# Kernel optimization log

Measured on AMD Instinct MI355X. Metric: run time of the kernel, lower is better.

Reference implementation:

```python
import jax, jax.numpy as jnp
import numpy as np


def squash(x, axis=-1):
    sq = jnp.sum(x * x, axis=axis, keepdims=True)
    return (sq / (1.0 + sq)) * (x / (jnp.sqrt(sq) + 1e-8))


def conv2d(x, w, b, stride):
    y = jax.lax.conv_general_dilated(x, w, (stride, stride), 'VALID',
                                     dimension_numbers=('NCHW', 'OIHW', 'NCHW'))
    return y + b[None, :, None, None]


def setup_inputs():
    key = jax.random.key(0)
    ks = jax.random.split(key, 8)
    B = 512
    return {
        'x': jax.random.uniform(ks[0], (B, 1, 28, 28), jnp.float32),
        'conv_w': 0.1 * jax.random.normal(ks[1], (256, 1, 9, 9), jnp.float32),
        'conv_b': jnp.zeros((256,), jnp.float32),
        'pc_w': 0.02 * jax.random.normal(ks[2], (256, 256, 9, 9), jnp.float32),
        'pc_b': jnp.zeros((256,), jnp.float32),
        'W_route': 0.01 * jax.random.normal(ks[3], (10, 1152, 16, 8), jnp.float32),
        'dec_w1': 0.05 * jax.random.normal(ks[4], (512, 160), jnp.float32),
        'dec_b1': jnp.zeros((512,), jnp.float32),
        'dec_w2': 0.05 * jax.random.normal(ks[5], (1024, 512), jnp.float32),
        'dec_b2': jnp.zeros((1024,), jnp.float32),
        'dec_w3': 0.05 * jax.random.normal(ks[6], (784, 1024), jnp.float32),
        'dec_b3': jnp.zeros((784,), jnp.float32),
    }


def capsnet_forward(x, conv_w, conv_b, pc_w, pc_b, W_route,
                    dec_w1, dec_b1, dec_w2, dec_b2, dec_w3, dec_b3,
                    num_routing=3):
    B = x.shape[0]
    # conv1 + relu: [B,1,28,28] -> [B,256,20,20]
    h = jax.nn.relu(conv2d(x, conv_w, conv_b, 1))
    # primary caps conv: [B,256,20,20] -> [B,256,6,6]
    p = conv2d(h, pc_w, pc_b, 2)
    # reshape (C,H,W flattened, grouped by capsule dim 8) -> [B,1152,8], squash
    caps = squash(p.reshape(B, -1, 8))
    # u_hat[b,o,n,d] = sum_i W[o,n,d,i] * caps[b,n,i]  -> [B,10,1152,16]
    u_hat = jnp.einsum('ondi,bni->bond', W_route, caps)
    u_hat_d = jax.lax.stop_gradient(u_hat)
    # dynamic routing
    b_logit = jnp.zeros((B, 10, 1152), u_hat.dtype)
    for _ in range(num_routing - 1):
        c = jax.nn.softmax(b_logit, axis=1)              # over out caps
        s = jnp.einsum('bond,bon->bod', u_hat_d, c)      # [B,10,16]
        v = squash(s)
        b_logit = b_logit + jnp.einsum('bond,bod->bon', u_hat_d, v)
    c = jax.nn.softmax(b_logit, axis=1)
    s = jnp.einsum('bond,bon->bod', u_hat, c)
    v = squash(s)                                        # [B,10,16]
    logits = jnp.linalg.norm(v, axis=-1)                 # [B,10]
    pred = jax.nn.one_hot(jnp.argmax(logits, axis=-1), 10, dtype=v.dtype)
    dec_in = (v * pred[..., None]).reshape(B, -1)        # [B,160]
    h1 = jax.nn.relu(dec_in @ dec_w1.T + dec_b1)
    h2 = jax.nn.relu(h1 @ dec_w2.T + dec_b2)
    reconstruction = jax.nn.sigmoid(h2 @ dec_w3.T + dec_b3)
    return logits, reconstruction


def reference(x, conv_w, conv_b, pc_w, pc_b, W_route,
              dec_w1, dec_b1, dec_w2, dec_b2, dec_w3, dec_b3):
    return capsnet_forward(x, conv_w, conv_b, pc_w, pc_b, W_route,
                           dec_w1, dec_b1, dec_w2, dec_b2, dec_w3, dec_b3)
```

## Files before the change

kernel.cpp:

```cpp
#include <hip/hip_runtime.h>
#include <math.h>


typedef _Float16 f16x8 __attribute__((ext_vector_type(8)));
typedef float f32x4 __attribute__((ext_vector_type(4)));

__global__ __launch_bounds__(256) void k_conv1(const float* __restrict__ x,
        const float* __restrict__ w, const float* __restrict__ bias,
        _Float16* __restrict__ ahi, _Float16* __restrict__ alo) {
    __shared__ __align__(16) float xs[784];
    const int b = blockIdx.x;
    const int t = threadIdx.x;
    for (int i = t; i < 784; i += 256) xs[i] = x[b * 784 + i];
    __syncthreads();

    float wr[81];
#pragma unroll
    for (int i = 0; i < 81; ++i) wr[i] = w[t * 81 + i];
    const float bv = bias[t];

    for (int oy = 0; oy < 20; ++oy) {
        float acc[20];
#pragma unroll
        for (int px = 0; px < 20; ++px) acc[px] = bv;
#pragma unroll
        for (int ky = 0; ky < 9; ++ky) {
            const float* xrow = &xs[(oy + ky) * 28];
            float xr[28];
#pragma unroll
            for (int j = 0; j < 7; ++j) {
                float4 v4 = *(const float4*)(xrow + j * 4);
                xr[j * 4 + 0] = v4.x; xr[j * 4 + 1] = v4.y;
                xr[j * 4 + 2] = v4.z; xr[j * 4 + 3] = v4.w;
            }
#pragma unroll
            for (int kx = 0; kx < 9; ++kx) {
                const float wv = wr[ky * 9 + kx];
#pragma unroll
                for (int px = 0; px < 20; ++px)
                    acc[px] = fmaf(wv, xr[px + kx], acc[px]);
            }
        }
#pragma unroll
        for (int px = 0; px < 20; ++px) {
            const float v16 = fmaxf(acc[px], 0.f) * 16.f;
            const _Float16 hi = (_Float16)v16;
            const _Float16 lo = (_Float16)(v16 - (float)hi);
            const int idx = (b * 400 + oy * 20 + px) * 256 + t;
            ahi[idx] = hi;
            alo[idx] = lo;
        }
    }
}

__global__ __launch_bounds__(256) void k_wcvt(const float* __restrict__ w2,
        _Float16* __restrict__ whi, _Float16* __restrict__ wlo) {
    const int i = blockIdx.x * 256 + threadIdx.x;
    const int n = i / 20736;
    const int r = i - n * 20736;
    const int tap = r >> 8;
    const int ci = r & 255;
    const float v = w2[(n * 256 + ci) * 81 + tap] * 16.f;
    const _Float16 hi = (_Float16)v;
    whi[i] = hi;
    wlo[i] = (_Float16)(v - (float)hi);
}

__global__ __launch_bounds__(256) void k_pinit(const float* __restrict__ bias,
        float* __restrict__ p) {
    const int idx = blockIdx.x * 256 + threadIdx.x;
    const int q = idx / 36;
    p[idx] = bias[q & 255];
}

__global__ __launch_bounds__(256, 2) void k_conv2m(
        const _Float16* __restrict__ ahi, const _Float16* __restrict__ alo,
        const _Float16* __restrict__ whi, const _Float16* __restrict__ wlo,
        float* __restrict__ p) {
    __shared__ __align__(16) _Float16 lds[32768];
    _Float16* sAhi = lds;
    _Float16* sAlo = lds + 8192;
    _Float16* sBhi = lds + 16384;
    _Float16* sBlo = lds + 24576;

    const int t = threadIdx.x;
    const int l = t & 63, w = t >> 6;
    const int m0 = blockIdx.x * 128;
    const int n0 = blockIdx.y * 128;
    const int kz = blockIdx.z;

    const int oct = ((t & 7) ^ ((t >> 3) & 7)) * 8;
    int apix[4], wbase[4];
#pragma unroll
    for (int i = 0; i < 4; ++i) {
        const int r = i * 32 + (t >> 3);
        const int m = m0 + r;
        const int b = m / 36, pix = m - b * 36;
        const int oy = pix / 6, ox = pix - oy * 6;
        apix[i] = (b * 400 + oy * 40 + ox * 2) * 256 + oct;
        wbase[i] = (n0 + r) * 20736 + oct;
    }

    f32x4 acc[4][4];
#pragma unroll
    for (int mf = 0; mf < 4; ++mf)
#pragma unroll
        for (int nf = 0; nf < 4; ++nf) acc[mf][nf] = (f32x4){0.f, 0.f, 0.f, 0.f};

    const int wm = (w >> 1) * 64, wn = (w & 1) * 64;
    const int lm = l & 15, lk = l >> 4;

    f16x8 rAh[4], rAl[4], rBh[4], rBl[4];

#define C2_LOAD(s) do { \
        const int tap_ = (s) >> 2; \
        const int ci0_ = ((s) & 3) << 6; \
        const int ky_ = tap_ / 9, kx_ = tap_ - ky_ * 9; \
        const int koff_ = (ky_ * 20 + kx_) * 256 + ci0_; \
        const int k0_ = (s) * 64; \
        _Pragma("unroll") \
        for (int i_ = 0; i_ < 4; ++i_) { \
            rAh[i_] = *(const f16x8*)(ahi + apix[i_] + koff_); \
            rAl[i_] = *(const f16x8*)(alo + apix[i_] + koff_); \
            rBh[i_] = *(const f16x8*)(whi + wbase[i_] + k0_); \
            rBl[i_] = *(const f16x8*)(wlo + wbase[i_] + k0_); \
        } \
    } while (0)

    C2_LOAD(kz);

    for (int j = 0; j < 162; ++j) {
        __syncthreads();
#pragma unroll
        for (int i = 0; i < 4; ++i) {
            *(f16x8*)(sAhi + i * 2048 + t * 8) = rAh[i];
            *(f16x8*)(sAlo + i * 2048 + t * 8) = rAl[i];
            *(f16x8*)(sBhi + i * 2048 + t * 8) = rBh[i];
            *(f16x8*)(sBlo + i * 2048 + t * 8) = rBl[i];
        }
        __syncthreads();
        if (j < 161) C2_LOAD(2 * (j + 1) + kz);

#pragma unroll
        for (int ks = 0; ks < 2; ++ks) {
            f16x8 afh[4], afl[4];
#pragma unroll
            for (int mf = 0; mf < 4; ++mf) {
                const int row = wm + mf * 16 + lm;
                const int off = row * 64 + ((ks * 4 + lk) ^ (lm & 7)) * 8;
                afh[mf] = *(const f16x8*)&sAhi[off];
                afl[mf] = *(const f16x8*)&sAlo[off];
            }
#pragma unroll
            for (int nf = 0; nf < 4; ++nf) {
                const int row = wn + nf * 16 + lm;
                const int off = row * 64 + ((ks * 4 + lk) ^ (lm & 7)) * 8;
                const f16x8 bh = *(const f16x8*)&sBhi[off];
                const f16x8 bl = *(const f16x8*)&sBlo[off];
#pragma unroll
                for (int mf = 0; mf < 4; ++mf) {
                    acc[mf][nf] = __builtin_amdgcn_mfma_f32_16x16x32_f16(
                        afh[mf], bh, acc[mf][nf], 0, 0, 0);
                    acc[mf][nf] = __builtin_amdgcn_mfma_f32_16x16x32_f16(
                        afh[mf], bl, acc[mf][nf], 0, 0, 0);
                    acc[mf][nf] = __builtin_amdgcn_mfma_f32_16x16x32_f16(
                        afl[mf], bh, acc[mf][nf], 0, 0, 0);
                }
            }
        }
    }
#undef C2_LOAD

#pragma unroll
    for (int nf = 0; nf < 4; ++nf) {
        const int n = n0 + wn + nf * 16 + lm;
#pragma unroll
        for (int mf = 0; mf < 4; ++mf) {
#pragma unroll
            for (int r = 0; r < 4; ++r) {
                const int m = m0 + wm + mf * 16 + lk * 4 + r;
                const int b = m / 36, pix = m - b * 36;
                atomicAdd(&p[(b * 256 + n) * 36 + pix],
                          acc[mf][nf][r] * (1.f / 256.f));
            }
        }
    }
}

__global__ __launch_bounds__(256) void k_squash(float* __restrict__ pc) {
    const long long i = (long long)blockIdx.x * 256 + threadIdx.x;
    float* p = pc + i * 8;
    float4 v0 = *(float4*)p;
    float4 v1 = *(float4*)(p + 4);
    const float sq = v0.x * v0.x + v0.y * v0.y + v0.z * v0.z + v0.w * v0.w
                   + v1.x * v1.x + v1.y * v1.y + v1.z * v1.z + v1.w * v1.w;
    const float sc = (sq / (1.f + sq)) / (sqrtf(sq) + 1e-8f);
    v0.x *= sc; v0.y *= sc; v0.z *= sc; v0.w *= sc;
    v1.x *= sc; v1.y *= sc; v1.z *= sc; v1.w *= sc;
    *(float4*)p = v0;
    *(float4*)(p + 4) = v1;
}

__global__ __launch_bounds__(128) void k_route(const float* __restrict__ caps,
        const float* __restrict__ W, const float* __restrict__ vsum,
        float* __restrict__ sp, int uniform) {
    const int b = blockIdx.x, nc = blockIdx.y;
    const int t = threadIdx.x;
    const int d = t & 15, g = t >> 4;
    __shared__ float vs[160];
    __shared__ float red[2][160];
    if (uniform == 0)
        for (int i = t; i < 160; i += 128) vs[i] = vsum[b * 160 + i];
    __syncthreads();

    float sacc[10];
#pragma unroll
    for (int o = 0; o < 10; ++o) sacc[o] = 0.f;

    for (int i = 0; i < 16; ++i) {
        const int n = nc * 128 + i * 8 + g;
        const float* cp = caps + ((long long)b * 1152 + n) * 8;
        const float4 ca = *(const float4*)cp;
        const float4 cb = *(const float4*)(cp + 4);
        float uv[10];
#pragma unroll
        for (int o = 0; o < 10; ++o) {
            const float* wp = W + (((long long)o * 1152 + n) * 16 + d) * 8;
            const float4 wa = *(const float4*)wp;
            const float4 wb = *(const float4*)(wp + 4);
            float s = wa.x * ca.x;
            s = fmaf(wa.y, ca.y, s); s = fmaf(wa.z, ca.z, s); s = fmaf(wa.w, ca.w, s);
            s = fmaf(wb.x, cb.x, s); s = fmaf(wb.y, cb.y, s); s = fmaf(wb.z, cb.z, s);
            s = fmaf(wb.w, cb.w, s);
            uv[o] = s;
        }
        float c[10];
        if (uniform) {
#pragma unroll
            for (int o = 0; o < 10; ++o) c[o] = 0.1f;
        } else {
            float dot[10];
#pragma unroll
            for (int o = 0; o < 10; ++o) {
                float xx = uv[o] * vs[o * 16 + d];
                xx += __shfl_xor(xx, 1);
                xx += __shfl_xor(xx, 2);
                xx += __shfl_xor(xx, 4);
                xx += __shfl_xor(xx, 8);
                dot[o] = xx;
            }
            float mx = dot[0];
#pragma unroll
            for (int o = 1; o < 10; ++o) mx = fmaxf(mx, dot[o]);
            float sum = 0.f;
#pragma unroll
            for (int o = 0; o < 10; ++o) { c[o] = expf(dot[o] - mx); sum += c[o]; }
            const float inv = 1.f / sum;
#pragma unroll
            for (int o = 0; o < 10; ++o) c[o] *= inv;
        }
#pragma unroll
        for (int o = 0; o < 10; ++o) sacc[o] = fmaf(c[o], uv[o], sacc[o]);
    }
#pragma unroll
    for (int o = 0; o < 10; ++o) {
        sacc[o] += __shfl_xor(sacc[o], 16);
        sacc[o] += __shfl_xor(sacc[o], 32);
    }
    const int wv = t >> 6;
    if ((t & 63) < 16) {
#pragma unroll
        for (int o = 0; o < 10; ++o) red[wv][o * 16 + d] = sacc[o];
    }
    __syncthreads();
    for (int i = t; i < 160; i += 128)
        sp[((long long)(b * 9 + nc)) * 160 + i] = red[0][i] + red[1][i];
}

__global__ __launch_bounds__(160) void k_squashv(const float* __restrict__ sp,
        float* __restrict__ vsum, float* __restrict__ vbuf, int first) {
    const int b = blockIdx.x, t = threadIdx.x;
    float s = 0.f;
#pragma unroll
    for (int ch = 0; ch < 9; ++ch) s += sp[((long long)(b * 9 + ch)) * 160 + t];
    float sq = s * s;
    sq += __shfl_xor(sq, 1);
    sq += __shfl_xor(sq, 2);
    sq += __shfl_xor(sq, 4);
    sq += __shfl_xor(sq, 8);
    const float sc = (sq / (1.f + sq)) / (sqrtf(sq) + 1e-8f);
    const float v = s * sc;
    vbuf[b * 160 + t] = v;
    vsum[b * 160 + t] = first ? v : (vsum[b * 160 + t] + v);
}

__global__ __launch_bounds__(64) void k_logits(const float* __restrict__ v,
        float* __restrict__ logits, float* __restrict__ dec_in) {
    const int b = blockIdx.x * 64 + threadIdx.x;
    const float* vp = v + (long long)b * 160;
    float nrm[10];
    int amax = 0;
    float best = -1.f;
#pragma unroll
    for (int o = 0; o < 10; ++o) {
        float s = 0.f;
#pragma unroll
        for (int dd = 0; dd < 16; ++dd) { const float xv = vp[o * 16 + dd]; s = fmaf(xv, xv, s); }
        nrm[o] = sqrtf(s);
        if (nrm[o] > best) { best = nrm[o]; amax = o; }
    }
#pragma unroll
    for (int o = 0; o < 10; ++o) logits[b * 10 + o] = nrm[o];
#pragma unroll
    for (int o = 0; o < 10; ++o)
#pragma unroll
        for (int dd = 0; dd < 16; ++dd)
            dec_in[(long long)b * 160 + o * 16 + dd] = (o == amax) ? vp[o * 16 + dd] : 0.f;
}

template <int ACT>
__global__ __launch_bounds__(256) void k_gemm(const float* __restrict__ A,
        const float* __restrict__ W, const float* __restrict__ bias,
        float* __restrict__ C, int N, int K) {
    __shared__ float As[16][68];
    __shared__ float Bs[16][68];
    const int m0 = blockIdx.x * 64, n0 = blockIdx.y * 64;
    const int t = threadIdx.x;
    const int kl = t & 15, rr = t >> 4;
    const int tm = t & 15, tn = t >> 4;

    float acc[4][4];
#pragma unroll
    for (int i = 0; i < 4; ++i)
#pragma unroll
        for (int j = 0; j < 4; ++j) acc[i][j] = 0.f;

    for (int k0 = 0; k0 < K; k0 += 16) {
#pragma unroll
        for (int i = 0; i < 4; ++i) {
            As[kl][rr + i * 16] = A[(m0 + rr + i * 16) * K + k0 + kl];
            const int n = n0 + rr + i * 16;
            Bs[kl][rr + i * 16] = (n < N) ? W[(long long)n * K + k0 + kl] : 0.f;
        }
        __syncthreads();
#pragma unroll
        for (int kk = 0; kk < 16; ++kk) {
            float a[4], bb[4];
#pragma unroll
            for (int i = 0; i < 4; ++i) a[i] = As[kk][tm * 4 + i];
#pragma unroll
            for (int j = 0; j < 4; ++j) bb[j] = Bs[kk][tn * 4 + j];
#pragma unroll
            for (int i = 0; i < 4; ++i)
#pragma unroll
                for (int j = 0; j < 4; ++j)
                    acc[i][j] = fmaf(a[i], bb[j], acc[i][j]);
        }
        __syncthreads();
    }
#pragma unroll
    for (int j = 0; j < 4; ++j) {
        const int n = n0 + tn * 4 + j;
        if (n < N) {
            const float bv = bias[n];
#pragma unroll
            for (int i = 0; i < 4; ++i) {
                const int m = m0 + tm * 4 + i;
                float xv = acc[i][j] + bv;
                if (ACT == 0) xv = fmaxf(xv, 0.f);
                else          xv = 1.f / (1.f + expf(-xv));
                C[(long long)m * N + n] = xv;
            }
        }
    }
}

extern "C" void kernel_launch(void* const* d_in, const int* in_sizes, int n_in,
                              void* d_out, int out_size, void* d_ws, size_t ws_size,
                              hipStream_t stream) {
    const float* x      = (const float*)d_in[0];
    const float* conv_w = (const float*)d_in[1];
    const float* conv_b = (const float*)d_in[2];
    const float* pc_w   = (const float*)d_in[3];
    const float* pc_b   = (const float*)d_in[4];
    const float* Wrt    = (const float*)d_in[5];
    const float* dw1    = (const float*)d_in[6];
    const float* db1    = (const float*)d_in[7];
    const float* dw2    = (const float*)d_in[8];
    const float* db2    = (const float*)d_in[9];
    const float* dw3    = (const float*)d_in[10];
    const float* db3    = (const float*)d_in[11];

    float* out = (float*)d_out;
    char* wsb  = (char*)d_ws;

    _Float16* ahi = (_Float16*)(wsb);
    _Float16* alo = (_Float16*)(wsb + 104857600);
    _Float16* whi = (_Float16*)(wsb + 209715200);
    _Float16* wlo = (_Float16*)(wsb + 220332032);
    float* caps = (float*)(wsb + 230948864);
    float* spart= (float*)(wsb);
    float* vsum = (float*)(wsb + 2949120);
    float* vbuf = (float*)(wsb + 3276800);
    float* din  = (float*)(wsb + 3604480);
    float* h1   = (float*)(wsb + 3932160);
    float* h2   = (float*)(wsb + 4980736);

    k_conv1<<<512, 256, 0, stream>>>(x, conv_w, conv_b, ahi, alo);
    k_wcvt<<<20736, 256, 0, stream>>>(pc_w, whi, wlo);
    k_pinit<<<18432, 256, 0, stream>>>(pc_b, caps);
    k_conv2m<<<dim3(144, 2, 2), 256, 0, stream>>>(ahi, alo, whi, wlo, caps);
    k_squash<<<2304, 256, 0, stream>>>(caps);

    k_route<<<dim3(512, 9), 128, 0, stream>>>(caps, Wrt, vsum, spart, 1);
    k_squashv<<<512, 160, 0, stream>>>(spart, vsum, vbuf, 1);
    k_route<<<dim3(512, 9), 128, 0, stream>>>(caps, Wrt, vsum, spart, 0);
    k_squashv<<<512, 160, 0, stream>>>(spart, vsum, vbuf, 0);
    k_route<<<dim3(512, 9), 128, 0, stream>>>(caps, Wrt, vsum, spart, 0);
    k_squashv<<<512, 160, 0, stream>>>(spart, vsum, vbuf, 0);

    k_logits<<<8, 64, 0, stream>>>(vbuf, out, din);

    k_gemm<0><<<dim3(8, 8),  256, 0, stream>>>(din, dw1, db1, h1, 512, 160);
    k_gemm<0><<<dim3(8, 16), 256, 0, stream>>>(h1,  dw2, db2, h2, 1024, 512);
    k_gemm<1><<<dim3(8, 13), 256, 0, stream>>>(h2,  dw3, db3, out + 5120, 784, 1024);
}
```

Baseline: 1.715 ms.

## Split conv1 rows across blocks, halve conv2 K-tile, restructure routing to reuse W in LDS

```diff
diff --git a/kernel.cpp b/kernel.cpp
--- a/kernel.cpp
+++ b/kernel.cpp
@@ -10,6 +10,7 @@
         _Float16* __restrict__ ahi, _Float16* __restrict__ alo) {
     __shared__ __align__(16) float xs[784];
     const int b = blockIdx.x;
+    const int oy0 = blockIdx.y * 4;
     const int t = threadIdx.x;
     for (int i = t; i < 784; i += 256) xs[i] = x[b * 784 + i];
     __syncthreads();
@@ -19,7 +20,7 @@
     for (int i = 0; i < 81; ++i) wr[i] = w[t * 81 + i];
     const float bv = bias[t];
 
-    for (int oy = 0; oy < 20; ++oy) {
+    for (int oy = oy0; oy < oy0 + 4; ++oy) {
         float acc[20];
 #pragma unroll
         for (int px = 0; px < 20; ++px) acc[px] = bv;
@@ -73,32 +74,34 @@
     p[idx] = bias[q & 255];
 }
 
-__global__ __launch_bounds__(256, 2) void k_conv2m(
+__global__ __launch_bounds__(256, 3) void k_conv2m(
         const _Float16* __restrict__ ahi, const _Float16* __restrict__ alo,
         const _Float16* __restrict__ whi, const _Float16* __restrict__ wlo,
         float* __restrict__ p) {
-    __shared__ __align__(16) _Float16 lds[32768];
+    __shared__ __align__(16) _Float16 lds[16384];
     _Float16* sAhi = lds;
-    _Float16* sAlo = lds + 8192;
-    _Float16* sBhi = lds + 16384;
-    _Float16* sBlo = lds + 24576;
+    _Float16* sAlo = lds + 4096;
+    _Float16* sBhi = lds + 8192;
+    _Float16* sBlo = lds + 12288;
 
     const int t = threadIdx.x;
     const int l = t & 63, w = t >> 6;
+    const int lm = l & 15, lk = l >> 4;
     const int m0 = blockIdx.x * 128;
     const int n0 = blockIdx.y * 128;
     const int kz = blockIdx.z;
 
-    const int oct = ((t & 7) ^ ((t >> 3) & 7)) * 8;
-    int apix[4], wbase[4];
-#pragma unroll
-    for (int i = 0; i < 4; ++i) {
-        const int r = i * 32 + (t >> 3);
-        const int m = m0 + r;
+    int abase[2], bbase[2];
+#pragma unroll
+    for (int i = 0; i < 2; ++i) {
+        const int slot = i * 256 + t;
+        const int row = slot >> 2, phys = slot & 3;
+        const int logk = phys ^ ((row >> 1) & 3);
+        const int m = m0 + row;
         const int b = m / 36, pix = m - b * 36;
         const int oy = pix / 6, ox = pix - oy * 6;
-        apix[i] = (b * 400 + oy * 40 + ox * 2) * 256 + oct;
-        wbase[i] = (n0 + r) * 20736 + oct;
+        abase[i] = (b * 400 + oy * 40 + ox * 2) * 256 + logk * 8;
+        bbase[i] = (n0 + row) * 20736 + logk * 8;
     }
 
     f32x4 acc[4][4];
@@ -108,68 +111,64 @@
         for (int nf = 0; nf < 4; ++nf) acc[mf][nf] = (f32x4){0.f, 0.f, 0.f, 0.f};
 
     const int wm = (w >> 1) * 64, wn = (w & 1) * 64;
-    const int lm = l & 15, lk = l >> 4;
-
-    f16x8 rAh[4], rAl[4], rBh[4], rBl[4];
-
-#define C2_LOAD(s) do { \
-        const int tap_ = (s) >> 2; \
-        const int ci0_ = ((s) & 3) << 6; \
-        const int ky_ = tap_ / 9, kx_ = tap_ - ky_ * 9; \
-        const int koff_ = (ky_ * 20 + kx_) * 256 + ci0_; \
-        const int k0_ = (s) * 64; \
-        _Pragma("unroll") \
-        for (int i_ = 0; i_ < 4; ++i_) { \
-            rAh[i_] = *(const f16x8*)(ahi + apix[i_] + koff_); \
-            rAl[i_] = *(const f16x8*)(alo + apix[i_] + koff_); \
-            rBh[i_] = *(const f16x8*)(whi + wbase[i_] + k0_); \
-            rBl[i_] = *(const f16x8*)(wlo + wbase[i_] + k0_); \
-        } \
+
+    f16x8 rAh[2], rAl[2], rBh[2], rBl[2];
+
+#define KOFFA(s_) (((((s_) >> 3) / 9) * 20 + (((s_) >> 3) % 9)) * 256 + (((s_) & 7) << 5))
+#define LOAD(s_) do { \
+        const int ka_ = KOFFA(s_), kb_ = (s_) * 32; \
+        rAh[0] = *(const f16x8*)(ahi + abase[0] + ka_); \
+        rAl[0] = *(const f16x8*)(alo + abase[0] + ka_); \
+        rAh[1] = *(const f16x8*)(ahi + abase[1] + ka_); \
+        rAl[1] = *(const f16x8*)(alo + abase[1] + ka_); \
+        rBh[0] = *(const f16x8*)(whi + bbase[0] + kb_); \
+        rBl[0] = *(const f16x8*)(wlo + bbase[0] + kb_); \
+        rBh[1] = *(const f16x8*)(whi + bbase[1] + kb_); \
+        rBl[1] = *(const f16x8*)(wlo + bbase[1] + kb_); \
     } while (0)
 
-    C2_LOAD(kz);
-
-    for (int j = 0; j < 162; ++j) {
+    LOAD(kz);
+
+    for (int j = 0; j < 324; ++j) {
         __syncthreads();
-#pragma unroll
-        for (int i = 0; i < 4; ++i) {
-            *(f16x8*)(sAhi + i * 2048 + t * 8) = rAh[i];
-            *(f16x8*)(sAlo + i * 2048 + t * 8) = rAl[i];
-            *(f16x8*)(sBhi + i * 2048 + t * 8) = rBh[i];
-            *(f16x8*)(sBlo + i * 2048 + t * 8) = rBl[i];
-        }
+        *(f16x8*)(sAhi + t * 8)        = rAh[0];
+        *(f16x8*)(sAhi + 2048 + t * 8) = rAh[1];
+        *(f16x8*)(sAlo + t * 8)        = rAl[0];
+        *(f16x8*)(sAlo + 2048 + t * 8) = rAl[1];
+        *(f16x8*)(sBhi + t * 8)        = rBh[0];
+        *(f16x8*)(sBhi + 2048 + t * 8) = rBh[1];
+        *(f16x8*)(sBlo + t * 8)        = rBl[0];
+        *(f16x8*)(sBlo + 2048 + t * 8) = rBl[1];
         __syncthreads();
-        if (j < 161) C2_LOAD(2 * (j + 1) + kz);
-
-#pragma unroll
-        for (int ks = 0; ks < 2; ++ks) {
-            f16x8 afh[4], afl[4];
+        if (j < 323) LOAD(2 * (j + 1) + kz);
+
+        f16x8 afh[4], afl[4];
+#pragma unroll
+        for (int mf = 0; mf < 4; ++mf) {
+            const int row = wm + mf * 16 + lm;
+            const int off = (row * 4 + (lk ^ ((row >> 1) & 3))) * 8;
+            afh[mf] = *(const f16x8*)&sAhi[off];
+            afl[mf] = *(const f16x8*)&sAlo[off];
+        }
+#pragma unroll
+        for (int nf = 0; nf < 4; ++nf) {
+            const int row = wn + nf * 16 + lm;
+            const int off = (row * 4 + (lk ^ ((row >> 1) & 3))) * 8;
+            const f16x8 bh = *(const f16x8*)&sBhi[off];
+            const f16x8 bl = *(const f16x8*)&sBlo[off];
 #pragma unroll
             for (int mf = 0; mf < 4; ++mf) {
-                const int row = wm + mf * 16 + lm;
-                const int off = row * 64 + ((ks * 4 + lk) ^ (lm & 7)) * 8;
-                afh[mf] = *(const f16x8*)&sAhi[off];
-                afl[mf] = *(const f16x8*)&sAlo[off];
-            }
-#pragma unroll
-            for (int nf = 0; nf < 4; ++nf) {
-                const int row = wn + nf * 16 + lm;
-                const int off = row * 64 + ((ks * 4 + lk) ^ (lm & 7)) * 8;
-                const f16x8 bh = *(const f16x8*)&sBhi[off];
-                const f16x8 bl = *(const f16x8*)&sBlo[off];
-#pragma unroll
-                for (int mf = 0; mf < 4; ++mf) {
-                    acc[mf][nf] = __builtin_amdgcn_mfma_f32_16x16x32_f16(
-                        afh[mf], bh, acc[mf][nf], 0, 0, 0);
-                    acc[mf][nf] = __builtin_amdgcn_mfma_f32_16x16x32_f16(
-                        afh[mf], bl, acc[mf][nf], 0, 0, 0);
-                    acc[mf][nf] = __builtin_amdgcn_mfma_f32_16x16x32_f16(
-                        afl[mf], bh, acc[mf][nf], 0, 0, 0);
-                }
-            }
-        }
-    }
-#undef C2_LOAD
+                acc[mf][nf] = __builtin_amdgcn_mfma_f32_16x16x32_f16(
+                    afh[mf], bh, acc[mf][nf], 0, 0, 0);
+                acc[mf][nf] = __builtin_amdgcn_mfma_f32_16x16x32_f16(
+                    afh[mf], bl, acc[mf][nf], 0, 0, 0);
+                acc[mf][nf] = __builtin_amdgcn_mfma_f32_16x16x32_f16(
+                    afl[mf], bh, acc[mf][nf], 0, 0, 0);
+            }
+        }
+    }
+#undef LOAD
+#undef KOFFA
 
 #pragma unroll
     for (int nf = 0; nf < 4; ++nf) {
@@ -201,88 +200,110 @@
     *(float4*)(p + 4) = v1;
 }
 
-__global__ __launch_bounds__(128) void k_route(const float* __restrict__ caps,
+__global__ __launch_bounds__(256, 2) void k_route(const float* __restrict__ caps,
         const float* __restrict__ W, const float* __restrict__ vsum,
         float* __restrict__ sp, int uniform) {
-    const int b = blockIdx.x, nc = blockIdx.y;
+    __shared__ __align__(16) float Wl[10240];
+    const int nc = blockIdx.x, bc = blockIdx.y;
     const int t = threadIdx.x;
     const int d = t & 15, g = t >> 4;
-    __shared__ float vs[160];
-    __shared__ float red[2][160];
-    if (uniform == 0)
-        for (int i = t; i < 160; i += 128) vs[i] = vsum[b * 160 + i];
+    const int n0 = nc * 8;
+
+#pragma unroll
+    for (int ii = 0; ii < 10; ++ii) {
+        const int idx = (ii * 256 + t) * 4;
+        const int o = idx >> 10;
+        *(float4*)&Wl[idx] =
+            *(const float4*)(W + o * 147456 + n0 * 128 + (idx & 1023));
+    }
     __syncthreads();
 
-    float sacc[10];
-#pragma unroll
-    for (int o = 0; o < 10; ++o) sacc[o] = 0.f;
-
-    for (int i = 0; i < 16; ++i) {
-        const int n = nc * 128 + i * 8 + g;
-        const float* cp = caps + ((long long)b * 1152 + n) * 8;
-        const float4 ca = *(const float4*)cp;
-        const float4 cb = *(const float4*)(cp + 4);
-        float uv[10];
+    float vs[4][10];
+    if (!uniform) {
+#pragma unroll
+        for (int j = 0; j < 4; ++j) {
+            const int b = bc * 64 + j * 16 + g;
+#pragma unroll
+            for (int o = 0; o < 10; ++o)
+                vs[j][o] = vsum[b * 160 + o * 16 + d];
+        }
+    }
+
+    float sacc[4][10];
+#pragma unroll
+    for (int j = 0; j < 4; ++j)
+#pragma unroll
+        for (int o = 0; o < 10; ++o) sacc[j][o] = 0.f;
+
+    for (int n = 0; n < 8; ++n) {
+        float4 wva[10], wvb[10];
 #pragma unroll
         for (int o = 0; o < 10; ++o) {
-            const float* wp = W + (((long long)o * 1152 + n) * 16 + d) * 8;
-            const float4 wa = *(const float4*)wp;
-            const float4 wb = *(const float4*)(wp + 4);
-            float s = wa.x * ca.x;
-            s = fmaf(wa.y, ca.y, s); s = fmaf(wa.z, ca.z, s); s = fmaf(wa.w, ca.w, s);
-            s = fmaf(wb.x, cb.x, s); s = fmaf(wb.y, cb.y, s); s = fmaf(wb.z, cb.z, s);
-            s = fmaf(wb.w, cb.w, s);
-            uv[o] = s;
-        }
-        float c[10];
-        if (uniform) {
-#pragma unroll
-            for (int o = 0; o < 10; ++o) c[o] = 0.1f;
-        } else {
-            float dot[10];
+            const float* wp = &Wl[((o * 8 + n) * 16 + d) * 8];
+            wva[o] = *(const float4*)wp;
+            wvb[o] = *(const float4*)(wp + 4);
+        }
+#pragma unroll
+        for (int j = 0; j < 4; ++j) {
+            const int b = bc * 64 + j * 16 + g;
+            const float* cp = caps + ((long long)b * 1152 + n0 + n) * 8;
+            const float4 ca = *(const float4*)cp;
+            const float4 cb = *(const float4*)(cp + 4);
+            float uv[10];
 #pragma unroll
             for (int o = 0; o < 10; ++o) {
-                float xx = uv[o] * vs[o * 16 + d];
-                xx += __shfl_xor(xx, 1);
-                xx += __shfl_xor(xx, 2);
-                xx += __shfl_xor(xx, 4);
-                xx += __shfl_xor(xx, 8);
-                dot[o] = xx;
-            }
-            float mx = dot[0];
-#pragma unroll
-            for (int o = 1; o < 10; ++o) mx = fmaxf(mx, dot[o]);
-            float sum = 0.f;
-#pragma unroll
-            for (int o = 0; o < 10; ++o) { c[o] = expf(dot[o] - mx); sum += c[o]; }
-            const float inv = 1.f / sum;
-#pragma unroll
-            for (int o = 0; o < 10; ++o) c[o] *= inv;
-        }
-#pragma unroll
-        for (int o = 0; o < 10; ++o) sacc[o] = fmaf(c[o], uv[o], sacc[o]);
-    }
-#pragma unroll
-    for (int o = 0; o < 10; ++o) {
-        sacc[o] += __shfl_xor(sacc[o], 16);
-        sacc[o] += __shfl_xor(sacc[o], 32);
-    }
-    const int wv = t >> 6;
-    if ((t & 63) < 16) {
-#pragma unroll
-        for (int o = 0; o < 10; ++o) red[wv][o * 16 + d] = sacc[o];
-    }
-    __syncthreads();
-    for (int i = t; i < 160; i += 128)
-        sp[((long long)(b * 9 + nc)) * 160 + i] = red[0][i] + red[1][i];
+                float s = wva[o].x * ca.x;
+                s = fmaf(wva[o].y, ca.y, s); s = fmaf(wva[o].z, ca.z, s);
+                s = fmaf(wva[o].w, ca.w, s);
+                s = fmaf(wvb[o].x, cb.x, s); s = fmaf(wvb[o].y, cb.y, s);
+                s = fmaf(wvb[o].z, cb.z, s); s = fmaf(wvb[o].w, cb.w, s);
+                uv[o] = s;
+            }
+            float c[10];
+            if (uniform) {
+#pragma unroll
+                for (int o = 0; o < 10; ++o) c[o] = 0.1f;
+            } else {
+                float dot[10];
+#pragma unroll
+                for (int o = 0; o < 10; ++o) {
+                    float xx = uv[o] * vs[j][o];
+                    xx += __shfl_xor(xx, 1);
+                    xx += __shfl_xor(xx, 2);
+                    xx += __shfl_xor(xx, 4);
+                    xx += __shfl_xor(xx, 8);
+                    dot[o] = xx;
+                }
+                float mx = dot[0];
+#pragma unroll
+                for (int o = 1; o < 10; ++o) mx = fmaxf(mx, dot[o]);
+                float sum = 0.f;
+#pragma unroll
+                for (int o = 0; o < 10; ++o) { c[o] = expf(dot[o] - mx); sum += c[o]; }
+                const float inv = 1.f / sum;
+#pragma unroll
+                for (int o = 0; o < 10; ++o) c[o] *= inv;
+            }
+#pragma unroll
+            for (int o = 0; o < 10; ++o)
+                sacc[j][o] = fmaf(c[o], uv[o], sacc[j][o]);
+        }
+    }
+#pragma unroll
+    for (int j = 0; j < 4; ++j) {
+        const int b = bc * 64 + j * 16 + g;
+#pragma unroll
+        for (int o = 0; o < 10; ++o)
+            sp[((long long)b * 144 + nc) * 160 + o * 16 + d] = sacc[j][o];
+    }
 }
 
 __global__ __launch_bounds__(160) void k_squashv(const float* __restrict__ sp,
         float* __restrict__ vsum, float* __restrict__ vbuf, int first) {
     const int b = blockIdx.x, t = threadIdx.x;
     float s = 0.f;
-#pragma unroll
-    for (int ch = 0; ch < 9; ++ch) s += sp[((long long)(b * 9 + ch)) * 160 + t];
+    for (int ch = 0; ch < 144; ++ch)
+        s += sp[((long long)b * 144 + ch) * 160 + t];
     float sq = s * s;
     sq += __shfl_xor(sq, 1);
     sq += __shfl_xor(sq, 2);
@@ -400,23 +421,23 @@
     _Float16* wlo = (_Float16*)(wsb + 220332032);
     float* caps = (float*)(wsb + 230948864);
     float* spart= (float*)(wsb);
-    float* vsum = (float*)(wsb + 2949120);
-    float* vbuf = (float*)(wsb + 3276800);
-    float* din  = (float*)(wsb + 3604480);
-    float* h1   = (float*)(wsb + 3932160);
-    float* h2   = (float*)(wsb + 4980736);
-
-    k_conv1<<<512, 256, 0, stream>>>(x, conv_w, conv_b, ahi, alo);
+    float* vsum = (float*)(wsb + 47185920);
+    float* vbuf = (float*)(wsb + 47513600);
+    float* din  = (float*)(wsb + 47841280);
+    float* h1   = (float*)(wsb + 48168960);
+    float* h2   = (float*)(wsb + 49217536);
+
+    k_conv1<<<dim3(512, 5), 256, 0, stream>>>(x, conv_w, conv_b, ahi, alo);
     k_wcvt<<<20736, 256, 0, stream>>>(pc_w, whi, wlo);
     k_pinit<<<18432, 256, 0, stream>>>(pc_b, caps);
     k_conv2m<<<dim3(144, 2, 2), 256, 0, stream>>>(ahi, alo, whi, wlo, caps);
     k_squash<<<2304, 256, 0, stream>>>(caps);
 
-    k_route<<<dim3(512, 9), 128, 0, stream>>>(caps, Wrt, vsum, spart, 1);
+    k_route<<<dim3(144, 8), 256, 0, stream>>>(caps, Wrt, vsum, spart, 1);
     k_squashv<<<512, 160, 0, stream>>>(spart, vsum, vbuf, 1);
-    k_route<<<dim3(512, 9), 128, 0, stream>>>(caps, Wrt, vsum, spart, 0);
+    k_route<<<dim3(144, 8), 256, 0, stream>>>(caps, Wrt, vsum, spart, 0);
     k_squashv<<<512, 160, 0, stream>>>(spart, vsum, vbuf, 0);
-    k_route<<<dim3(512, 9), 128, 0, stream>>>(caps, Wrt, vsum, spart, 0);
+    k_route<<<dim3(144, 8), 256, 0, stream>>>(caps, Wrt, vsum, spart, 0);
     k_squashv<<<512, 160, 0, stream>>>(spart, vsum, vbuf, 0);
 
     k_logits<<<8, 64, 0, stream>>>(vbuf, out, din);
```

Result: no change. 1.734 ms (+1.1%).
